# Optimization experiments

Hardware: AMD Instinct MI355X
Metric: run time of the kernel (lower is better)

## Reference

```python
import jax, jax.numpy as jnp
import numpy as np

B, T, D, E, C = 4, 4096, 2048, 8, 1024
H = D // E  # per-expert hidden = out_features // num_experts = 256


def setup_inputs() -> dict:
    key = jax.random.key(0)
    ks = jax.random.split(key, 7)
    x = jax.random.normal(ks[0], (B, T, D), dtype=jnp.float32)
    # nn.Linear-style init scale ~ 1/sqrt(fan_in)
    W1 = jax.random.normal(ks[1], (E, H, D), dtype=jnp.float32) / np.sqrt(D)
    b1 = jax.random.normal(ks[2], (E, H), dtype=jnp.float32) / np.sqrt(D)
    W2 = jax.random.normal(ks[3], (E, D, H), dtype=jnp.float32) / np.sqrt(D)
    b2 = jax.random.normal(ks[4], (D,), dtype=jnp.float32) / np.sqrt(D)
    expert_indices = jax.random.randint(ks[5], (B, E, C), 0, T, dtype=jnp.int32)
    expert_gate = jax.random.uniform(ks[6], (B, E, C), dtype=jnp.float32)
    return {"x": x, "W1": W1, "b1": b1, "W2": W2, "b2": b2,
            "expert_indices": expert_indices, "expert_gate": expert_gate,
            "num_tokens": T}


def reference(x, W1, b1, W2, b2, expert_indices, expert_gate, num_tokens):
    # x: (B,T,D); expert_indices/expert_gate: (B,E,C)
    Bb = x.shape[0]
    Ee, Cc = expert_indices.shape[1], expert_indices.shape[2]
    b_idx = jnp.arange(Bb)[:, None, None]
    # dispatch: gather tokens per expert -> (B,E,C,D)
    sel = x[b_idx, expert_indices]
    # contract: per-expert GEMM -> (B,E,C,H)
    h = jnp.einsum('becd,ehd->bech', sel, W1) + b1[None, :, None, :]
    h = jax.nn.gelu(h, approximate=False)
    # expand: per-expert GEMM -> (B,E,C,D), shared output bias
    y = jnp.einsum('bech,eoh->beco', h, W2) + b2
    y = y * expert_gate[..., None]
    # combine: gated scatter-add back to token positions -> (B,T,D)
    out = jnp.zeros((Bb, num_tokens, x.shape[2]), dtype=x.dtype)
    out = out.at[jnp.arange(Bb)[:, None], expert_indices.reshape(Bb, Ee * Cc)].add(
        y.reshape(Bb, Ee * Cc, -1))
    return out
```

## Files before the change

### kernel.cpp

```cpp
#include <hip/hip_runtime.h>
#include <math.h>

#define B_ 4
#define T_ 4096
#define D_ 2048
#define E_ 8
#define C_ 1024
#define H_ 256
#define SLOTCAP 32

typedef unsigned short u16;
typedef unsigned long long u64;
typedef __attribute__((ext_vector_type(8))) short short8;
typedef __attribute__((ext_vector_type(4))) float f32x4;

__device__ __forceinline__ u16 f2bf(float f) {
    union { float f; unsigned u; } v; v.f = f;
    unsigned r = (v.u + 0x7FFFu + ((v.u >> 16) & 1u)) >> 16;
    return (u16)r;
}
__device__ __forceinline__ float bf2f(u16 u) {
    union { unsigned u; float f; } v; v.u = ((unsigned)u) << 16;
    return v.f;
}

__device__ __forceinline__ int swz(int row, int chunk) {
    return (row << 6) + ((chunk ^ (row & 7)) << 3);
}

__global__ __launch_bounds__(256) void conv_f32_bf16(
    const float* __restrict__ src, u16* __restrict__ dst, int n)
{
    int i = (blockIdx.x * 256 + threadIdx.x) * 4;
    if (i >= n) return;
    f32x4 v = *reinterpret_cast<const f32x4*>(src + i);
    u16 o[4];
    o[0] = f2bf(v[0]); o[1] = f2bf(v[1]); o[2] = f2bf(v[2]); o[3] = f2bf(v[3]);
    *reinterpret_cast<u64*>(dst + i) = *reinterpret_cast<const u64*>(o);
}

__global__ __launch_bounds__(512) void gemm1_v2(
    const float* __restrict__ x, const u16* __restrict__ W1bf,
    const float* __restrict__ b1, const int* __restrict__ idx,
    u16* __restrict__ Hbuf)
{
    const int mt = blockIdx.x;
    const int be = blockIdx.y;
    const int b = be >> 3, e = be & 7;
    const int m0 = mt * 128;

    __shared__ __align__(16) u16 As[128 * 64];
    __shared__ __align__(16) u16 Bs[256 * 64];
    __shared__ int toks[128];
    __shared__ float bs1[256];

    const int tid = threadIdx.x;
    if (tid < 128) toks[tid] = idx[(b * E_ + e) * C_ + m0 + tid];
    if (tid < 256) bs1[tid] = b1[e * H_ + tid];
    __syncthreads();

    const int lane = tid & 63, wid = tid >> 6;
    const int wm = wid >> 2, wn = wid & 3;
    const int l15 = lane & 15, lk = lane >> 4;

    const int ar = tid >> 2, ac0 = tid & 3;
    const float* aRow = x + (size_t)b * (T_ * (size_t)D_)
                          + (size_t)toks[ar] * D_;
    const int br = tid >> 1, bc0 = (tid & 1) * 4;
    const u16* bRow = W1bf + ((size_t)e * H_ + br) * D_;

    const int aOff0 = swz(ar, ac0), aOff1 = swz(ar, ac0 + 4);
    int bOff[4];
    #pragma unroll
    for (int j = 0; j < 4; ++j) bOff[j] = swz(br, bc0 + j);

    f32x4 acc[4][4];
    #pragma unroll
    for (int i = 0; i < 4; ++i)
        #pragma unroll
        for (int j = 0; j < 4; ++j)
            acc[i][j] = (f32x4){0.f, 0.f, 0.f, 0.f};

    f32x4 pa[4];
    short8 pb[4];

    pa[0] = *reinterpret_cast<const f32x4*>(aRow + ac0 * 8);
    pa[1] = *reinterpret_cast<const f32x4*>(aRow + ac0 * 8 + 4);
    pa[2] = *reinterpret_cast<const f32x4*>(aRow + (ac0 + 4) * 8);
    pa[3] = *reinterpret_cast<const f32x4*>(aRow + (ac0 + 4) * 8 + 4);
    #pragma unroll
    for (int j = 0; j < 4; ++j)
        pb[j] = *reinterpret_cast<const short8*>(bRow + (bc0 + j) * 8);
    {
        short8 s0, s1;
        #pragma unroll
        for (int r = 0; r < 4; ++r) {
            s0[r] = (short)f2bf(pa[0][r]); s0[r + 4] = (short)f2bf(pa[1][r]);
            s1[r] = (short)f2bf(pa[2][r]); s1[r + 4] = (short)f2bf(pa[3][r]);
        }
        *reinterpret_cast<short8*>(&As[aOff0]) = s0;
        *reinterpret_cast<short8*>(&As[aOff1]) = s1;
        #pragma unroll
        for (int j = 0; j < 4; ++j)
            *reinterpret_cast<short8*>(&Bs[bOff[j]]) = pb[j];
    }
    __syncthreads();

    const int NT = D_ / 64;
    for (int t = 0; t < NT; ++t) {
        if (t + 1 < NT) {
            const int k = (t + 1) * 64;
            pa[0] = *reinterpret_cast<const f32x4*>(aRow + k + ac0 * 8);
            pa[1] = *reinterpret_cast<const f32x4*>(aRow + k + ac0 * 8 + 4);
            pa[2] = *reinterpret_cast<const f32x4*>(aRow + k + (ac0 + 4) * 8);
            pa[3] = *reinterpret_cast<const f32x4*>(aRow + k + (ac0 + 4) * 8 + 4);
            #pragma unroll
            for (int j = 0; j < 4; ++j)
                pb[j] = *reinterpret_cast<const short8*>(bRow + k + (bc0 + j) * 8);
        }
        #pragma unroll
        for (int kk = 0; kk < 2; ++kk) {
            short8 af[4], bfr[4];
            #pragma unroll
            for (int m = 0; m < 4; ++m) {
                const int row = wm * 64 + m * 16 + l15;
                af[m] = *reinterpret_cast<const short8*>(&As[swz(row, kk * 4 + lk)]);
            }
            #pragma unroll
            for (int n = 0; n < 4; ++n) {
                const int row = wn * 64 + n * 16 + l15;
                bfr[n] = *reinterpret_cast<const short8*>(&Bs[swz(row, kk * 4 + lk)]);
            }
            #pragma unroll
            for (int m = 0; m < 4; ++m)
                #pragma unroll
                for (int n = 0; n < 4; ++n)
                    acc[m][n] = __builtin_amdgcn_mfma_f32_16x16x32_bf16(
                        bfr[n], af[m], acc[m][n], 0, 0, 0);
        }
        if (t + 1 < NT) {
            __syncthreads();
            short8 s0, s1;
            #pragma unroll
            for (int r = 0; r < 4; ++r) {
                s0[r] = (short)f2bf(pa[0][r]); s0[r + 4] = (short)f2bf(pa[1][r]);
                s1[r] = (short)f2bf(pa[2][r]); s1[r + 4] = (short)f2bf(pa[3][r]);
            }
            *reinterpret_cast<short8*>(&As[aOff0]) = s0;
            *reinterpret_cast<short8*>(&As[aOff1]) = s1;
            #pragma unroll
            for (int j = 0; j < 4; ++j)
                *reinterpret_cast<short8*>(&Bs[bOff[j]]) = pb[j];
            __syncthreads();
        }
    }

    const size_t hbase = ((size_t)(b * E_ + e) * C_ + m0) * H_;
    #pragma unroll
    for (int m = 0; m < 4; ++m) {
        const int cl = wm * 64 + m * 16 + l15;
        u16* rowp = Hbuf + hbase + (size_t)cl * H_;
        #pragma unroll
        for (int n = 0; n < 4; ++n) {
            const int hb = wn * 64 + n * 16 + lk * 4;
            u16 o[4];
            #pragma unroll
            for (int r = 0; r < 4; ++r) {
                float h = acc[m][n][r] + bs1[hb + r];
                float g = 0.5f * h * (1.0f + erff(h * 0.70710678118f));
                o[r] = f2bf(g);
            }
            *reinterpret_cast<u64*>(rowp + hb) = *reinterpret_cast<const u64*>(o);
        }
    }
}

__global__ __launch_bounds__(512) void gemm2_v2(
    const u16* __restrict__ Hbuf, const u16* __restrict__ W2bf,
    const float* __restrict__ b2, const float* __restrict__ gate,
    u16* __restrict__ Ybuf)
{
    const int mt = blockIdx.x >> 3, nt = blockIdx.x & 7;
    const int be = blockIdx.y;
    const int b = be >> 3, e = be & 7;
    const int m0 = mt * 128, n0 = nt * 256;

    __shared__ __align__(16) u16 As[128 * 64];
    __shared__ __align__(16) u16 Bs[256 * 64];
    __shared__ float gs[128];
    __shared__ float bs2[256];

    const int tid = threadIdx.x;
    if (tid < 128) gs[tid] = gate[(b * E_ + e) * C_ + m0 + tid];
    if (tid < 256) bs2[tid] = b2[n0 + tid];
    __syncthreads();

    const int lane = tid & 63, wid = tid >> 6;
    const int wm = wid >> 2, wn = wid & 3;
    const int l15 = lane & 15, lk = lane >> 4;

    const int ar = tid >> 2, ac0 = tid & 3;
    const u16* aRow = Hbuf + ((size_t)(b * E_ + e) * C_ + m0 + ar) * H_;
    const int br = tid >> 1, bc0 = (tid & 1) * 4;
    const u16* bRow = W2bf + ((size_t)e * D_ + n0 + br) * H_;

    const int aOff0 = swz(ar, ac0), aOff1 = swz(ar, ac0 + 4);
    int bOff[4];
    #pragma unroll
    for (int j = 0; j < 4; ++j) bOff[j] = swz(br, bc0 + j);

    f32x4 acc[4][4];
    #pragma unroll
    for (int i = 0; i < 4; ++i)
        #pragma unroll
        for (int j = 0; j < 4; ++j)
            acc[i][j] = (f32x4){0.f, 0.f, 0.f, 0.f};

    short8 pa0, pa1, pb[4];
    pa0 = *reinterpret_cast<const short8*>(aRow + ac0 * 8);
    pa1 = *reinterpret_cast<const short8*>(aRow + (ac0 + 4) * 8);
    #pragma unroll
    for (int j = 0; j < 4; ++j)
        pb[j] = *reinterpret_cast<const short8*>(bRow + (bc0 + j) * 8);
    *reinterpret_cast<short8*>(&As[aOff0]) = pa0;
    *reinterpret_cast<short8*>(&As[aOff1]) = pa1;
    #pragma unroll
    for (int j = 0; j < 4; ++j)
        *reinterpret_cast<short8*>(&Bs[bOff[j]]) = pb[j];
    __syncthreads();

    const int NT = H_ / 64;
    for (int t = 0; t < NT; ++t) {
        if (t + 1 < NT) {
            const int k = (t + 1) * 64;
            pa0 = *reinterpret_cast<const short8*>(aRow + k + ac0 * 8);
            pa1 = *reinterpret_cast<const short8*>(aRow + k + (ac0 + 4) * 8);
            #pragma unroll
            for (int j = 0; j < 4; ++j)
                pb[j] = *reinterpret_cast<const short8*>(bRow + k + (bc0 + j) * 8);
        }
        #pragma unroll
        for (int kk = 0; kk < 2; ++kk) {
            short8 af[4], bfr[4];
            #pragma unroll
            for (int m = 0; m < 4; ++m) {
                const int row = wm * 64 + m * 16 + l15;
                af[m] = *reinterpret_cast<const short8*>(&As[swz(row, kk * 4 + lk)]);
            }
            #pragma unroll
            for (int n = 0; n < 4; ++n) {
                const int row = wn * 64 + n * 16 + l15;
                bfr[n] = *reinterpret_cast<const short8*>(&Bs[swz(row, kk * 4 + lk)]);
            }
            #pragma unroll
            for (int m = 0; m < 4; ++m)
                #pragma unroll
                for (int n = 0; n < 4; ++n)
                    acc[m][n] = __builtin_amdgcn_mfma_f32_16x16x32_bf16(
                        bfr[n], af[m], acc[m][n], 0, 0, 0);
        }
        if (t + 1 < NT) {
            __syncthreads();
            *reinterpret_cast<short8*>(&As[aOff0]) = pa0;
            *reinterpret_cast<short8*>(&As[aOff1]) = pa1;
            #pragma unroll
            for (int j = 0; j < 4; ++j)
                *reinterpret_cast<short8*>(&Bs[bOff[j]]) = pb[j];
            __syncthreads();
        }
    }

    const size_t ybase = (size_t)(b * E_ + e) * C_ + m0;
    #pragma unroll
    for (int m = 0; m < 4; ++m) {
        const int cl = wm * 64 + m * 16 + l15;
        const float g = gs[cl];
        u16* rowp = Ybuf + (ybase + cl) * (size_t)D_ + n0;
        #pragma unroll
        for (int n = 0; n < 4; ++n) {
            const int db = wn * 64 + n * 16 + lk * 4;
            u16 o[4];
            #pragma unroll
            for (int r = 0; r < 4; ++r)
                o[r] = f2bf((acc[m][n][r] + bs2[db + r]) * g);
            *reinterpret_cast<u64*>(rowp + db) = *reinterpret_cast<const u64*>(o);
        }
    }
}

__global__ __launch_bounds__(256) void fill_kernel(
    const int* __restrict__ idx, int* __restrict__ cnt,
    int* __restrict__ slots)
{
    int i = blockIdx.x * 256 + threadIdx.x;
    if (i >= B_ * E_ * C_) return;
    int b = i / (E_ * C_);
    int slot = i % (E_ * C_);
    int t = idx[i];
    int p = atomicAdd(&cnt[b * T_ + t], 1);
    if (p < SLOTCAP) slots[(b * T_ + t) * SLOTCAP + p] = slot;
}

__global__ __launch_bounds__(256) void combine_kernel(
    const u16* __restrict__ Ybuf, const int* __restrict__ cnt,
    const int* __restrict__ slots, float* __restrict__ out)
{
    const int bt = blockIdx.x;
    const int tid = threadIdx.x;
    __shared__ int sl[SLOTCAP];
    int n = cnt[bt];
    n = n > SLOTCAP ? SLOTCAP : n;
    if (tid < n) sl[tid] = slots[bt * SLOTCAP + tid];
    __syncthreads();
    const int b = bt >> 12;
    float a[8] = {0.f, 0.f, 0.f, 0.f, 0.f, 0.f, 0.f, 0.f};
    for (int s = 0; s < n; ++s) {
        const u16* yrow = Ybuf + ((size_t)b * (E_ * C_) + sl[s]) * D_ + tid * 8;
        short8 v = *reinterpret_cast<const short8*>(yrow);
        #pragma unroll
        for (int j = 0; j < 8; ++j) a[j] += bf2f((u16)v[j]);
    }
    float* orow = out + (size_t)bt * D_ + tid * 8;
    *reinterpret_cast<f32x4*>(orow)     = (f32x4){a[0], a[1], a[2], a[3]};
    *reinterpret_cast<f32x4*>(orow + 4) = (f32x4){a[4], a[5], a[6], a[7]};
}

extern "C" void kernel_launch(void* const* d_in, const int* in_sizes, int n_in,
                              void* d_out, int out_size, void* d_ws, size_t ws_size,
                              hipStream_t stream) {
    const float* x    = (const float*)d_in[0];
    const float* W1   = (const float*)d_in[1];
    const float* b1   = (const float*)d_in[2];
    const float* W2   = (const float*)d_in[3];
    const float* b2   = (const float*)d_in[4];
    const int*   idx  = (const int*)d_in[5];
    const float* gate = (const float*)d_in[6];
    float* out = (float*)d_out;

    const size_t nW = (size_t)E_ * H_ * D_;
    const size_t nH = (size_t)B_ * E_ * C_ * H_;
    const size_t nY = (size_t)B_ * E_ * C_ * D_;

    u16* W1bf = (u16*)d_ws;
    u16* W2bf = W1bf + nW;
    u16* Hbuf = W2bf + nW;
    u16* Ybuf = Hbuf + nH;
    int* cnt   = (int*)(Ybuf + nY);
    int* slots = cnt + (size_t)B_ * T_;

    hipMemsetAsync(cnt, 0, (size_t)B_ * T_ * sizeof(int), stream);
    conv_f32_bf16<<<(int)(nW / 1024), 256, 0, stream>>>(W1, W1bf, (int)nW);
    conv_f32_bf16<<<(int)(nW / 1024), 256, 0, stream>>>(W2, W2bf, (int)nW);
    fill_kernel<<<(B_ * E_ * C_) / 256, 256, 0, stream>>>(idx, cnt, slots);

    gemm1_v2<<<dim3(8, 32), 512, 0, stream>>>(x, W1bf, b1, idx, Hbuf);
    gemm2_v2<<<dim3(64, 32), 512, 0, stream>>>(Hbuf, W2bf, b2, gate, Ybuf);
    combine_kernel<<<B_ * T_, 256, 0, stream>>>(Ybuf, cnt, slots, out);
}
```

Baseline: 244.3 us.

## Double-buffer LDS tiles in gemm1 with two-stage register prefetch

Gemm1 now keeps two LDS buffers for the A and B tiles. It writes the next tile into the alternate buffer before computing the current one and prefetches the tile two steps ahead into registers. This removes one of the two barriers per k-step and lets global loads and LDS stores overlap with MFMA work. In exchange LDS use doubles to about 96KB per block, which may reduce occupancy, and the raw waitcnt and barrier sequence needs careful ordering to stay correct.

```diff
diff --git a/kernel.cpp b/kernel.cpp
--- a/kernel.cpp
+++ b/kernel.cpp
@@ -39,7 +39,7 @@
     *reinterpret_cast<u64*>(dst + i) = *reinterpret_cast<const u64*>(o);
 }
 
-__global__ __launch_bounds__(512) void gemm1_v2(
+__global__ __launch_bounds__(512) void gemm1_v3(
     const float* __restrict__ x, const u16* __restrict__ W1bf,
     const float* __restrict__ b1, const int* __restrict__ idx,
     u16* __restrict__ Hbuf)
@@ -49,8 +49,8 @@
     const int b = be >> 3, e = be & 7;
     const int m0 = mt * 128;
 
-    __shared__ __align__(16) u16 As[128 * 64];
-    __shared__ __align__(16) u16 Bs[256 * 64];
+    __shared__ __align__(16) u16 As[2][128 * 64];
+    __shared__ __align__(16) u16 Bs[2][256 * 64];
     __shared__ int toks[128];
     __shared__ float bs1[256];
 
@@ -84,52 +84,57 @@
     f32x4 pa[4];
     short8 pb[4];
 
-    pa[0] = *reinterpret_cast<const f32x4*>(aRow + ac0 * 8);
-    pa[1] = *reinterpret_cast<const f32x4*>(aRow + ac0 * 8 + 4);
-    pa[2] = *reinterpret_cast<const f32x4*>(aRow + (ac0 + 4) * 8);
-    pa[3] = *reinterpret_cast<const f32x4*>(aRow + (ac0 + 4) * 8 + 4);
-    #pragma unroll
-    for (int j = 0; j < 4; ++j)
-        pb[j] = *reinterpret_cast<const short8*>(bRow + (bc0 + j) * 8);
-    {
-        short8 s0, s1;
-        #pragma unroll
-        for (int r = 0; r < 4; ++r) {
-            s0[r] = (short)f2bf(pa[0][r]); s0[r + 4] = (short)f2bf(pa[1][r]);
-            s1[r] = (short)f2bf(pa[2][r]); s1[r + 4] = (short)f2bf(pa[3][r]);
-        }
-        *reinterpret_cast<short8*>(&As[aOff0]) = s0;
-        *reinterpret_cast<short8*>(&As[aOff1]) = s1;
-        #pragma unroll
-        for (int j = 0; j < 4; ++j)
-            *reinterpret_cast<short8*>(&Bs[bOff[j]]) = pb[j];
-    }
-    __syncthreads();
+#define G1_LOAD(k)                                                            \
+    do {                                                                      \
+        pa[0] = *reinterpret_cast<const f32x4*>(aRow + (k) + ac0 * 8);        \
+        pa[1] = *reinterpret_cast<const f32x4*>(aRow + (k) + ac0 * 8 + 4);    \
+        pa[2] = *reinterpret_cast<const f32x4*>(aRow + (k) + (ac0 + 4) * 8);  \
+        pa[3] = *reinterpret_cast<const f32x4*>(aRow + (k) + (ac0 + 4) * 8 + 4);\
+        _Pragma("unroll")                                                     \
+        for (int j = 0; j < 4; ++j)                                           \
+            pb[j] = *reinterpret_cast<const short8*>(bRow + (k) + (bc0 + j) * 8);\
+    } while (0)
+
+#define G1_WRITE(buf)                                                         \
+    do {                                                                      \
+        short8 s0, s1;                                                        \
+        _Pragma("unroll")                                                     \
+        for (int r = 0; r < 4; ++r) {                                         \
+            s0[r] = (short)f2bf(pa[0][r]); s0[r + 4] = (short)f2bf(pa[1][r]); \
+            s1[r] = (short)f2bf(pa[2][r]); s1[r + 4] = (short)f2bf(pa[3][r]); \
+        }                                                                     \
+        *reinterpret_cast<short8*>(&As[buf][aOff0]) = s0;                     \
+        *reinterpret_cast<short8*>(&As[buf][aOff1]) = s1;                     \
+        _Pragma("unroll")                                                     \
+        for (int j = 0; j < 4; ++j)                                           \
+            *reinterpret_cast<short8*>(&Bs[buf][bOff[j]]) = pb[j];            \
+    } while (0)
+
+    G1_LOAD(0);
+    G1_WRITE(0);
+    G1_LOAD(64);
+    asm volatile("s_waitcnt lgkmcnt(0)" ::: "memory");
+    __builtin_amdgcn_s_barrier();
 
     const int NT = D_ / 64;
     for (int t = 0; t < NT; ++t) {
-        if (t + 1 < NT) {
-            const int k = (t + 1) * 64;
-            pa[0] = *reinterpret_cast<const f32x4*>(aRow + k + ac0 * 8);
-            pa[1] = *reinterpret_cast<const f32x4*>(aRow + k + ac0 * 8 + 4);
-            pa[2] = *reinterpret_cast<const f32x4*>(aRow + k + (ac0 + 4) * 8);
-            pa[3] = *reinterpret_cast<const f32x4*>(aRow + k + (ac0 + 4) * 8 + 4);
-            #pragma unroll
-            for (int j = 0; j < 4; ++j)
-                pb[j] = *reinterpret_cast<const short8*>(bRow + k + (bc0 + j) * 8);
-        }
+        const int cur = t & 1;
+        if (t + 1 < NT) G1_WRITE(cur ^ 1);
+        if (t + 2 < NT) G1_LOAD((t + 2) * 64);
         #pragma unroll
         for (int kk = 0; kk < 2; ++kk) {
             short8 af[4], bfr[4];
             #pragma unroll
             for (int m = 0; m < 4; ++m) {
                 const int row = wm * 64 + m * 16 + l15;
-                af[m] = *reinterpret_cast<const short8*>(&As[swz(row, kk * 4 + lk)]);
+                af[m] = *reinterpret_cast<const short8*>(
+                    &As[cur][swz(row, kk * 4 + lk)]);
             }
             #pragma unroll
             for (int n = 0; n < 4; ++n) {
                 const int row = wn * 64 + n * 16 + l15;
-                bfr[n] = *reinterpret_cast<const short8*>(&Bs[swz(row, kk * 4 + lk)]);
+                bfr[n] = *reinterpret_cast<const short8*>(
+                    &Bs[cur][swz(row, kk * 4 + lk)]);
             }
             #pragma unroll
             for (int m = 0; m < 4; ++m)
@@ -138,22 +143,11 @@
                     acc[m][n] = __builtin_amdgcn_mfma_f32_16x16x32_bf16(
                         bfr[n], af[m], acc[m][n], 0, 0, 0);
         }
-        if (t + 1 < NT) {
-            __syncthreads();
-            short8 s0, s1;
-            #pragma unroll
-            for (int r = 0; r < 4; ++r) {
-                s0[r] = (short)f2bf(pa[0][r]); s0[r + 4] = (short)f2bf(pa[1][r]);
-                s1[r] = (short)f2bf(pa[2][r]); s1[r + 4] = (short)f2bf(pa[3][r]);
-            }
-            *reinterpret_cast<short8*>(&As[aOff0]) = s0;
-            *reinterpret_cast<short8*>(&As[aOff1]) = s1;
-            #pragma unroll
-            for (int j = 0; j < 4; ++j)
-                *reinterpret_cast<short8*>(&Bs[bOff[j]]) = pb[j];
-            __syncthreads();
-        }
-    }
+        asm volatile("s_waitcnt lgkmcnt(0)" ::: "memory");
+        __builtin_amdgcn_s_barrier();
+    }
+#undef G1_LOAD
+#undef G1_WRITE
 
     const size_t hbase = ((size_t)(b * E_ + e) * C_ + m0) * H_;
     #pragma unroll
@@ -353,7 +347,7 @@
     conv_f32_bf16<<<(int)(nW / 1024), 256, 0, stream>>>(W2, W2bf, (int)nW);
     fill_kernel<<<(B_ * E_ * C_) / 256, 256, 0, stream>>>(idx, cnt, slots);
 
-    gemm1_v2<<<dim3(8, 32), 512, 0, stream>>>(x, W1bf, b1, idx, Hbuf);
+    gemm1_v3<<<dim3(8, 32), 512, 0, stream>>>(x, W1bf, b1, idx, Hbuf);
     gemm2_v2<<<dim3(64, 32), 512, 0, stream>>>(Hbuf, W2bf, b2, gate, Ybuf);
     combine_kernel<<<B_ * T_, 256, 0, stream>>>(Ybuf, cnt, slots, out);
 }
```

After: 219.0 us. 10.4% less time.
